# Performance work log

Hardware: AMD Instinct MI355X
Metric: run time of the kernel (lower is better)

Reference implementation:

```python
import jax, jax.numpy as jnp
import numpy as np

# ---- config constants (TwoCompartmentLIFConfig defaults) ----
DT = 1.0                      # ms per Euler step
G_L, E_L = 0.05, 0.0          # somatic leak
G_L_D = 0.03                  # dendritic leak
C_D = 0.5                     # dendritic capacitance
G_C = 0.05                    # soma-dendrite coupling
E_E, E_I = 3.0, -0.5
E_NMDA, E_GABA_B = 3.0, -0.8
E_CA = 4.0
E_ADAPT = -0.5
V_TH, V_RESET, TAU_REF = 1.0, 0.0, 5.0
MG_K, MG_VHALF = 5.0, 0.5     # NMDA Mg2+ block sigmoid
THETA_CA, G_CA_SPIKE = 2.0, 0.3
BAP_AMP = 0.3
ADAPT_INC = 0.0
# conductance decay factors exp(-dt/tau)
D_E  = float(np.exp(-DT / 5.0))
D_I  = float(np.exp(-DT / 10.0))
D_N  = float(np.exp(-DT / 100.0))
D_GB = float(np.exp(-DT / 400.0))
D_CA = float(np.exp(-DT / 20.0))
D_AD = float(np.exp(-DT / 100.0))

T, N = 50, 500000
IN_SCALE = 0.06


def setup_inputs() -> dict:
    key = jax.random.key(0)
    ks = jax.random.split(key, 7)
    names = ["g_exc_basal", "g_inh_basal", "g_nmda_basal", "g_gaba_b_in",
             "g_exc_apical", "g_inh_apical", "g_nmda_apical"]
    return {n: IN_SCALE * jax.random.uniform(k, (T, N), dtype=jnp.float32)
            for n, k in zip(names, ks)}


def _run(g_exc_basal, g_inh_basal, g_nmda_basal, g_gaba_b_in,
         g_exc_apical, g_inh_apical, g_nmda_apical):
    n = g_exc_basal.shape[1]
    z = jnp.zeros((n,), jnp.float32)
    # carry: v_soma, v_dend, gEb, gIb, gNb, gGB, gEa, gIa, gNa, gCa, gAd, ref
    carry0 = (z + E_L, z + E_L, z, z, z, z, z, z, z, z, z, z)

    def step(carry, inp):
        v_s, v_d, gEb, gIb, gNb, gGB, gEa, gIa, gNa, gCa, gAd, ref = carry
        in_Eb, in_Ib, in_Nb, in_GB, in_Ea, in_Ia, in_Na = inp
        # decay + inject synaptic conductances
        gEb = gEb * D_E + in_Eb
        gIb = gIb * D_I + in_Ib
        gNb = gNb * D_N + in_Nb
        gGB = gGB * D_GB + in_GB
        gEa = gEa * D_E + in_Ea
        gIa = gIa * D_I + in_Ia
        gNa = gNa * D_N + in_Na
        gCa = gCa * D_CA
        # NMDA Mg2+ block gated at the LOCAL compartment voltage
        mg_s = jax.nn.sigmoid(MG_K * (v_s - MG_VHALF))
        mg_d = jax.nn.sigmoid(MG_K * (v_d - MG_VHALF))
        # somatic current (C_m = 1)
        I_s = (G_L * (E_L - v_s) + gEb * (E_E - v_s) + gIb * (E_I - v_s)
               + gNb * mg_s * (E_NMDA - v_s) + gGB * (E_GABA_B - v_s)
               + gAd * (E_ADAPT - v_s) + G_C * (v_d - v_s))
        # dendritic current
        I_d = (G_L_D * (E_L - v_d) + gEa * (E_E - v_d) + gIa * (E_I - v_d)
               + gNa * mg_d * (E_NMDA - v_d) + gCa * (E_CA - v_d)
               + G_C * (v_s - v_d))
        refractory = ref > 0.0
        v_s = jnp.where(refractory, V_RESET, v_s + DT * I_s)
        v_d = v_d + (DT / C_D) * I_d
        # spike + reset + refractory
        spike = (v_s >= V_TH) & jnp.logical_not(refractory)
        spike_f = spike.astype(jnp.float32)
        v_s = jnp.where(spike, V_RESET, v_s)
        ref = jnp.where(spike, TAU_REF, jnp.maximum(ref - DT, 0.0))
        gAd = gAd * D_AD + spike_f * ADAPT_INC
        # back-propagating AP depolarises dendrite
        v_d = jnp.where(spike, v_d + BAP_AMP * (E_CA - v_d), v_d)
        # dendritic Ca spike
        gCa = gCa + (v_d >= THETA_CA).astype(jnp.float32) * G_CA_SPIKE
        carry = (v_s, v_d, gEb, gIb, gNb, gGB, gEa, gIa, gNa, gCa, gAd, ref)
        return carry, (spike_f, v_s)

    inputs = (g_exc_basal, g_inh_basal, g_nmda_basal, g_gaba_b_in,
              g_exc_apical, g_inh_apical, g_nmda_apical)
    _, (spikes, v_trace) = jax.lax.scan(step, carry0, inputs)
    return spikes, v_trace  # each [T, N]


def reference(g_exc_basal, g_inh_basal, g_nmda_basal, g_gaba_b_in,
              g_exc_apical, g_inh_apical, g_nmda_apical):
    return _run(g_exc_basal, g_inh_basal, g_nmda_basal, g_gaba_b_in,
                g_exc_apical, g_inh_apical, g_nmda_apical)
```

## Files before the change

kernel.cpp:

```cpp
#include <hip/hip_runtime.h>
#include <math.h>

namespace {
constexpr float D_E   = 0.8187307530779818f;
constexpr float D_I   = 0.9048374180359595f;
constexpr float D_N   = 0.9900498337491681f;
constexpr float D_GB  = 0.9975031223974601f;
constexpr float D_CA  = 0.9512294245007140f;

constexpr float DT      = 1.0f;
constexpr float G_L     = 0.05f;
constexpr float E_L     = 0.0f;
constexpr float G_L_D   = 0.03f;
constexpr float DT_C_D  = 2.0f;
constexpr float G_C     = 0.05f;
constexpr float E_E     = 3.0f;
constexpr float E_I     = -0.5f;
constexpr float E_NMDA  = 3.0f;
constexpr float E_GABA_B= -0.8f;
constexpr float E_CA    = 4.0f;
constexpr float V_TH    = 1.0f;
constexpr float V_RESET = 0.0f;
constexpr float TAU_REF = 5.0f;
constexpr float MG_K    = 5.0f;
constexpr float MG_VHALF= 0.5f;
constexpr float THETA_CA= 2.0f;
constexpr float G_CA_SPIKE = 0.3f;
constexpr float BAP_AMP = 0.3f;
}

typedef float f32x2 __attribute__((ext_vector_type(2)));

__device__ __forceinline__ float fast_sigmoid5(float v) {
    return __fdividef(1.0f, 1.0f + __expf(-MG_K * (v - MG_VHALF)));
}

struct State2 {
    float v_s[2], v_d[2];
    float gEb[2], gIb[2], gNb[2], gGB[2];
    float gEa[2], gIa[2], gNa[2], gCa[2], ref[2];
};

__device__ __forceinline__ void absorb2(
    const f32x2 iEb, const f32x2 iIb, const f32x2 iNb, const f32x2 iGB,
    const f32x2 iEa, const f32x2 iIa, const f32x2 iNa, State2& s)
{
    s.gEb[0] = s.gEb[0]*D_E  + iEb.x;  s.gEb[1] = s.gEb[1]*D_E  + iEb.y;
    s.gIb[0] = s.gIb[0]*D_I  + iIb.x;  s.gIb[1] = s.gIb[1]*D_I  + iIb.y;
    s.gNb[0] = s.gNb[0]*D_N  + iNb.x;  s.gNb[1] = s.gNb[1]*D_N  + iNb.y;
    s.gGB[0] = s.gGB[0]*D_GB + iGB.x;  s.gGB[1] = s.gGB[1]*D_GB + iGB.y;
    s.gEa[0] = s.gEa[0]*D_E  + iEa.x;  s.gEa[1] = s.gEa[1]*D_E  + iEa.y;
    s.gIa[0] = s.gIa[0]*D_I  + iIa.x;  s.gIa[1] = s.gIa[1]*D_I  + iIa.y;
    s.gNa[0] = s.gNa[0]*D_N  + iNa.x;  s.gNa[1] = s.gNa[1]*D_N  + iNa.y;
    s.gCa[0] *= D_CA;                  s.gCa[1] *= D_CA;
}

__device__ __forceinline__ void fire2(State2& s, f32x2& osp, f32x2& ov)
{
    #pragma unroll
    for (int j = 0; j < 2; ++j) {
        float v_s = s.v_s[j], v_d = s.v_d[j];
        const float mg_s = fast_sigmoid5(v_s);
        const float mg_d = fast_sigmoid5(v_d);
        const float I_s = G_L*(E_L - v_s) + s.gEb[j]*(E_E - v_s) + s.gIb[j]*(E_I - v_s)
                        + s.gNb[j]*mg_s*(E_NMDA - v_s) + s.gGB[j]*(E_GABA_B - v_s)
                        + G_C*(v_d - v_s);
        const float I_d = G_L_D*(E_L - v_d) + s.gEa[j]*(E_E - v_d) + s.gIa[j]*(E_I - v_d)
                        + s.gNa[j]*mg_d*(E_NMDA - v_d) + s.gCa[j]*(E_CA - v_d)
                        + G_C*(v_s - v_d);
        const bool refractory = s.ref[j] > 0.0f;
        v_s = refractory ? V_RESET : (v_s + DT*I_s);
        v_d = v_d + DT_C_D*I_d;
        const bool spike = (v_s >= V_TH) && !refractory;
        const float spike_f = spike ? 1.0f : 0.0f;
        v_s = spike ? V_RESET : v_s;
        s.ref[j] = spike ? TAU_REF : fmaxf(s.ref[j] - DT, 0.0f);
        v_d = spike ? (v_d + BAP_AMP*(E_CA - v_d)) : v_d;
        s.gCa[j] += (v_d >= THETA_CA) ? G_CA_SPIKE : 0.0f;
        s.v_s[j] = v_s; s.v_d[j] = v_d;
        if (j == 0) { osp.x = spike_f; ov.x = v_s; }
        else        { osp.y = spike_f; ov.y = v_s; }
    }
}

#define LOAD7(S, OFF)                                     \
    S##Eb = *(const f32x2*)(pEb + (OFF));                 \
    S##Ib = *(const f32x2*)(pIb + (OFF));                 \
    S##Nb = *(const f32x2*)(pNb + (OFF));                 \
    S##GB = *(const f32x2*)(pGB + (OFF));                 \
    S##Ea = *(const f32x2*)(pEa + (OFF));                 \
    S##Ia = *(const f32x2*)(pIa + (OFF));                 \
    S##Na = *(const f32x2*)(pNa + (OFF));

__global__ __launch_bounds__(256, 4)
void lif_f2_pf2_kernel(const float* __restrict__ pEb, const float* __restrict__ pIb,
                       const float* __restrict__ pNb, const float* __restrict__ pGB,
                       const float* __restrict__ pEa, const float* __restrict__ pIa,
                       const float* __restrict__ pNa,
                       float* __restrict__ out, int N, int T)
{
    const int tid = blockIdx.x * blockDim.x + threadIdx.x;
    const long long base = (long long)tid * 2;
    if (base >= N) return;

    State2 s;
    #pragma unroll
    for (int j = 0; j < 2; ++j) {
        s.v_s[j] = E_L; s.v_d[j] = E_L;
        s.gEb[j] = 0; s.gIb[j] = 0; s.gNb[j] = 0; s.gGB[j] = 0;
        s.gEa[j] = 0; s.gIa[j] = 0; s.gNa[j] = 0; s.gCa[j] = 0; s.ref[j] = 0;
    }

    const size_t vtr     = (size_t)T * (size_t)N;
    const size_t lastoff = (size_t)(T - 1) * (size_t)N + (size_t)base;

    size_t off = (size_t)base;
    f32x2 aEb, aIb, aNb, aGB, aEa, aIa, aNa;
    f32x2 bEb, bIb, bNb, bGB, bEa, bIa, bNa;
    LOAD7(a, off)
    LOAD7(b, off + (size_t)N)

    for (int t = 0; t < T; t += 2) {
        f32x2 osp, ov;

        absorb2(aEb, aIb, aNb, aGB, aEa, aIa, aNa, s);
        {
            const size_t la = (t + 2 < T) ? off + 2 * (size_t)N : lastoff;
            LOAD7(a, la)
        }
        fire2(s, osp, ov);
        __builtin_nontemporal_store(osp, reinterpret_cast<f32x2*>(out + off));
        __builtin_nontemporal_store(ov,  reinterpret_cast<f32x2*>(out + vtr + off));
        off += (size_t)N;

        absorb2(bEb, bIb, bNb, bGB, bEa, bIa, bNa, s);
        {
            const size_t lb = (t + 3 < T) ? off + 2 * (size_t)N : lastoff;
            LOAD7(b, lb)
        }
        fire2(s, osp, ov);
        __builtin_nontemporal_store(osp, reinterpret_cast<f32x2*>(out + off));
        __builtin_nontemporal_store(ov,  reinterpret_cast<f32x2*>(out + vtr + off));
        off += (size_t)N;
    }
}

__global__ __launch_bounds__(256, 8)
void lif_scalar_kernel(const float* __restrict__ pEb, const float* __restrict__ pIb,
                       const float* __restrict__ pNb, const float* __restrict__ pGB,
                       const float* __restrict__ pEa, const float* __restrict__ pIa,
                       const float* __restrict__ pNa,
                       float* __restrict__ out, int N, int T)
{
    const int i = blockIdx.x * blockDim.x + threadIdx.x;
    if (i >= N) return;
    State2 s;
    s.v_s[0] = E_L; s.v_d[0] = E_L;
    s.gEb[0] = 0; s.gIb[0] = 0; s.gNb[0] = 0; s.gGB[0] = 0;
    s.gEa[0] = 0; s.gIa[0] = 0; s.gNa[0] = 0; s.gCa[0] = 0; s.ref[0] = 0;
    s.v_s[1] = E_L; s.v_d[1] = E_L;
    s.gEb[1] = 0; s.gIb[1] = 0; s.gNb[1] = 0; s.gGB[1] = 0;
    s.gEa[1] = 0; s.gIa[1] = 0; s.gNa[1] = 0; s.gCa[1] = 0; s.ref[1] = 0;

    const size_t vtr = (size_t)T * (size_t)N;
    for (int t = 0; t < T; ++t) {
        const size_t off = (size_t)t * (size_t)N + (size_t)i;
        f32x2 iEb = {pEb[off], 0.0f}, iIb = {pIb[off], 0.0f};
        f32x2 iNb = {pNb[off], 0.0f}, iGB = {pGB[off], 0.0f};
        f32x2 iEa = {pEa[off], 0.0f}, iIa = {pIa[off], 0.0f};
        f32x2 iNa = {pNa[off], 0.0f};
        absorb2(iEb, iIb, iNb, iGB, iEa, iIa, iNa, s);
        f32x2 osp, ov;
        fire2(s, osp, ov);
        out[off]       = osp.x;
        out[vtr + off] = ov.x;
    }
}

extern "C" void kernel_launch(void* const* d_in, const int* in_sizes, int n_in,
                              void* d_out, int out_size, void* d_ws, size_t ws_size,
                              hipStream_t stream) {
    const float* pEb = (const float*)d_in[0];
    const float* pIb = (const float*)d_in[1];
    const float* pNb = (const float*)d_in[2];
    const float* pGB = (const float*)d_in[3];
    const float* pEa = (const float*)d_in[4];
    const float* pIa = (const float*)d_in[5];
    const float* pNa = (const float*)d_in[6];
    float* out = (float*)d_out;

    const int T = 50;
    const int N = in_sizes[0] / T;

    if ((N & 1) == 0 && (T & 1) == 0) {
        const int threads = N / 2;
        const int blocks = (threads + 255) / 256;
        lif_f2_pf2_kernel<<<blocks, 256, 0, stream>>>(pEb, pIb, pNb, pGB, pEa, pIa, pNa,
                                                      out, N, T);
    } else {
        const int blocks = (N + 255) / 256;
        lif_scalar_kernel<<<blocks, 256, 0, stream>>>(pEb, pIb, pNb, pGB, pEa, pIa, pNa,
                                                      out, N, T);
    }
}
```

Baseline: 174.5 us.

## Stream inputs through double-buffered LDS with direct global-to-LDS loads, 4 neurons per thread

Replaces the register-prefetch float2 kernel with one that issues 16-byte global_load_lds transfers of the next timestep's seven input rows into a double-buffered shared-memory tile, then reads them back as float4. Each thread now handles 4 neurons and writes float4 nontemporal stores. The aim is to raise bytes per memory instruction and let the asynchronous loads overlap compute without using prefetch registers. In exchange it adds a __syncthreads per timestep, drops the occupancy hint to 2 blocks, and clamps the tail block's addresses so lanes past N redundantly recompute and store the last 4 neurons.

```diff
diff --git a/kernel.cpp b/kernel.cpp
--- a/kernel.cpp
+++ b/kernel.cpp
@@ -1,5 +1,6 @@
 #include <hip/hip_runtime.h>
 #include <math.h>
+#include <stdint.h>
 
 namespace {
 constexpr float D_E   = 0.8187307530779818f;
@@ -29,36 +30,39 @@
 constexpr float BAP_AMP = 0.3f;
 }
 
-typedef float f32x2 __attribute__((ext_vector_type(2)));
+typedef float f32x4 __attribute__((ext_vector_type(4)));
 
 __device__ __forceinline__ float fast_sigmoid5(float v) {
     return __fdividef(1.0f, 1.0f + __expf(-MG_K * (v - MG_VHALF)));
 }
 
-struct State2 {
-    float v_s[2], v_d[2];
-    float gEb[2], gIb[2], gNb[2], gGB[2];
-    float gEa[2], gIa[2], gNa[2], gCa[2], ref[2];
+struct State4 {
+    float v_s[4], v_d[4];
+    float gEb[4], gIb[4], gNb[4], gGB[4];
+    float gEa[4], gIa[4], gNa[4], gCa[4], ref[4];
 };
 
-__device__ __forceinline__ void absorb2(
-    const f32x2 iEb, const f32x2 iIb, const f32x2 iNb, const f32x2 iGB,
-    const f32x2 iEa, const f32x2 iIa, const f32x2 iNa, State2& s)
-{
-    s.gEb[0] = s.gEb[0]*D_E  + iEb.x;  s.gEb[1] = s.gEb[1]*D_E  + iEb.y;
-    s.gIb[0] = s.gIb[0]*D_I  + iIb.x;  s.gIb[1] = s.gIb[1]*D_I  + iIb.y;
-    s.gNb[0] = s.gNb[0]*D_N  + iNb.x;  s.gNb[1] = s.gNb[1]*D_N  + iNb.y;
-    s.gGB[0] = s.gGB[0]*D_GB + iGB.x;  s.gGB[1] = s.gGB[1]*D_GB + iGB.y;
-    s.gEa[0] = s.gEa[0]*D_E  + iEa.x;  s.gEa[1] = s.gEa[1]*D_E  + iEa.y;
-    s.gIa[0] = s.gIa[0]*D_I  + iIa.x;  s.gIa[1] = s.gIa[1]*D_I  + iIa.y;
-    s.gNa[0] = s.gNa[0]*D_N  + iNa.x;  s.gNa[1] = s.gNa[1]*D_N  + iNa.y;
-    s.gCa[0] *= D_CA;                  s.gCa[1] *= D_CA;
-}
-
-__device__ __forceinline__ void fire2(State2& s, f32x2& osp, f32x2& ov)
+__device__ __forceinline__ void absorb4(
+    const f32x4 iEb, const f32x4 iIb, const f32x4 iNb, const f32x4 iGB,
+    const f32x4 iEa, const f32x4 iIa, const f32x4 iNa, State4& s)
 {
     #pragma unroll
-    for (int j = 0; j < 2; ++j) {
+    for (int j = 0; j < 4; ++j) {
+        s.gEb[j] = s.gEb[j]*D_E  + iEb[j];
+        s.gIb[j] = s.gIb[j]*D_I  + iIb[j];
+        s.gNb[j] = s.gNb[j]*D_N  + iNb[j];
+        s.gGB[j] = s.gGB[j]*D_GB + iGB[j];
+        s.gEa[j] = s.gEa[j]*D_E  + iEa[j];
+        s.gIa[j] = s.gIa[j]*D_I  + iIa[j];
+        s.gNa[j] = s.gNa[j]*D_N  + iNa[j];
+        s.gCa[j] *= D_CA;
+    }
+}
+
+__device__ __forceinline__ void fire4(State4& s, f32x4& osp, f32x4& ov)
+{
+    #pragma unroll
+    for (int j = 0; j < 4; ++j) {
         float v_s = s.v_s[j], v_d = s.v_d[j];
         const float mg_s = fast_sigmoid5(v_s);
         const float mg_d = fast_sigmoid5(v_d);
@@ -78,70 +82,77 @@
         v_d = spike ? (v_d + BAP_AMP*(E_CA - v_d)) : v_d;
         s.gCa[j] += (v_d >= THETA_CA) ? G_CA_SPIKE : 0.0f;
         s.v_s[j] = v_s; s.v_d[j] = v_d;
-        if (j == 0) { osp.x = spike_f; ov.x = v_s; }
-        else        { osp.y = spike_f; ov.y = v_s; }
-    }
-}
-
-#define LOAD7(S, OFF)                                     \
-    S##Eb = *(const f32x2*)(pEb + (OFF));                 \
-    S##Ib = *(const f32x2*)(pIb + (OFF));                 \
-    S##Nb = *(const f32x2*)(pNb + (OFF));                 \
-    S##GB = *(const f32x2*)(pGB + (OFF));                 \
-    S##Ea = *(const f32x2*)(pEa + (OFF));                 \
-    S##Ia = *(const f32x2*)(pIa + (OFF));                 \
-    S##Na = *(const f32x2*)(pNa + (OFF));
-
-__global__ __launch_bounds__(256, 4)
-void lif_f2_pf2_kernel(const float* __restrict__ pEb, const float* __restrict__ pIb,
-                       const float* __restrict__ pNb, const float* __restrict__ pGB,
-                       const float* __restrict__ pEa, const float* __restrict__ pIa,
-                       const float* __restrict__ pNa,
-                       float* __restrict__ out, int N, int T)
-{
-    const int tid = blockIdx.x * blockDim.x + threadIdx.x;
-    const long long base = (long long)tid * 2;
-    if (base >= N) return;
-
-    State2 s;
+        osp[j] = spike_f; ov[j] = v_s;
+    }
+}
+
+__global__ __launch_bounds__(256, 2)
+void lif_lds_kernel(const float* __restrict__ pEb, const float* __restrict__ pIb,
+                    const float* __restrict__ pNb, const float* __restrict__ pGB,
+                    const float* __restrict__ pEa, const float* __restrict__ pIa,
+                    const float* __restrict__ pNa,
+                    float* __restrict__ outSp, float* __restrict__ outV,
+                    int N, int T)
+{
+    __shared__ float lds[2][7][1024];
+    const int tid  = threadIdx.x;
+    const int wave = tid >> 6;
+    const float* in[7] = {pEb, pIb, pNb, pGB, pEa, pIa, pNa};
+
+    const long long b0  = (long long)blockIdx.x * 1024 + (long long)tid * 4;
+    const long long nm4 = (long long)N - 4;
+    const size_t gb = (size_t)(b0 < nm4 ? b0 : nm4);
+
+    {
+        #pragma unroll
+        for (int a = 0; a < 7; ++a)
+            __builtin_amdgcn_global_load_lds(
+                (const __attribute__((address_space(1))) uint32_t*)(in[a] + gb),
+                (__attribute__((address_space(3))) uint32_t*)&lds[0][a][wave * 256],
+                16, 0, 0);
+    }
+
+    State4 s;
     #pragma unroll
-    for (int j = 0; j < 2; ++j) {
+    for (int j = 0; j < 4; ++j) {
         s.v_s[j] = E_L; s.v_d[j] = E_L;
         s.gEb[j] = 0; s.gIb[j] = 0; s.gNb[j] = 0; s.gGB[j] = 0;
         s.gEa[j] = 0; s.gIa[j] = 0; s.gNa[j] = 0; s.gCa[j] = 0; s.ref[j] = 0;
     }
 
-    const size_t vtr     = (size_t)T * (size_t)N;
-    const size_t lastoff = (size_t)(T - 1) * (size_t)N + (size_t)base;
-
-    size_t off = (size_t)base;
-    f32x2 aEb, aIb, aNb, aGB, aEa, aIa, aNa;
-    f32x2 bEb, bIb, bNb, bGB, bEa, bIa, bNa;
-    LOAD7(a, off)
-    LOAD7(b, off + (size_t)N)
-
-    for (int t = 0; t < T; t += 2) {
-        f32x2 osp, ov;
-
-        absorb2(aEb, aIb, aNb, aGB, aEa, aIa, aNa, s);
-        {
-            const size_t la = (t + 2 < T) ? off + 2 * (size_t)N : lastoff;
-            LOAD7(a, la)
+    __syncthreads();
+
+    for (int t = 0; t < T; ++t) {
+        const int cur = t & 1;
+
+        if (t + 1 < T) {
+            const size_t row = (size_t)(t + 1) * (size_t)N + gb;
+            #pragma unroll
+            for (int a = 0; a < 7; ++a)
+                __builtin_amdgcn_global_load_lds(
+                    (const __attribute__((address_space(1))) uint32_t*)(in[a] + row),
+                    (__attribute__((address_space(3))) uint32_t*)&lds[cur ^ 1][a][wave * 256],
+                    16, 0, 0);
         }
-        fire2(s, osp, ov);
-        __builtin_nontemporal_store(osp, reinterpret_cast<f32x2*>(out + off));
-        __builtin_nontemporal_store(ov,  reinterpret_cast<f32x2*>(out + vtr + off));
-        off += (size_t)N;
-
-        absorb2(bEb, bIb, bNb, bGB, bEa, bIa, bNa, s);
-        {
-            const size_t lb = (t + 3 < T) ? off + 2 * (size_t)N : lastoff;
-            LOAD7(b, lb)
-        }
-        fire2(s, osp, ov);
-        __builtin_nontemporal_store(osp, reinterpret_cast<f32x2*>(out + off));
-        __builtin_nontemporal_store(ov,  reinterpret_cast<f32x2*>(out + vtr + off));
-        off += (size_t)N;
+
+        const int li = tid * 4;
+        const f32x4 iEb = *(const f32x4*)&lds[cur][0][li];
+        const f32x4 iIb = *(const f32x4*)&lds[cur][1][li];
+        const f32x4 iNb = *(const f32x4*)&lds[cur][2][li];
+        const f32x4 iGB = *(const f32x4*)&lds[cur][3][li];
+        const f32x4 iEa = *(const f32x4*)&lds[cur][4][li];
+        const f32x4 iIa = *(const f32x4*)&lds[cur][5][li];
+        const f32x4 iNa = *(const f32x4*)&lds[cur][6][li];
+
+        absorb4(iEb, iIb, iNb, iGB, iEa, iIa, iNa, s);
+        f32x4 osp, ov;
+        fire4(s, osp, ov);
+
+        const size_t o = (size_t)t * (size_t)N + gb;
+        __builtin_nontemporal_store(osp, (f32x4*)(outSp + o));
+        __builtin_nontemporal_store(ov,  (f32x4*)(outV  + o));
+
+        __syncthreads();
     }
 }
 
@@ -154,26 +165,40 @@
 {
     const int i = blockIdx.x * blockDim.x + threadIdx.x;
     if (i >= N) return;
-    State2 s;
-    s.v_s[0] = E_L; s.v_d[0] = E_L;
-    s.gEb[0] = 0; s.gIb[0] = 0; s.gNb[0] = 0; s.gGB[0] = 0;
-    s.gEa[0] = 0; s.gIa[0] = 0; s.gNa[0] = 0; s.gCa[0] = 0; s.ref[0] = 0;
-    s.v_s[1] = E_L; s.v_d[1] = E_L;
-    s.gEb[1] = 0; s.gIb[1] = 0; s.gNb[1] = 0; s.gGB[1] = 0;
-    s.gEa[1] = 0; s.gIa[1] = 0; s.gNa[1] = 0; s.gCa[1] = 0; s.ref[1] = 0;
-
+
+    float v_s = E_L, v_d = E_L;
+    float gEb = 0, gIb = 0, gNb = 0, gGB = 0;
+    float gEa = 0, gIa = 0, gNa = 0, gCa = 0, ref = 0;
     const size_t vtr = (size_t)T * (size_t)N;
+
     for (int t = 0; t < T; ++t) {
         const size_t off = (size_t)t * (size_t)N + (size_t)i;
-        f32x2 iEb = {pEb[off], 0.0f}, iIb = {pIb[off], 0.0f};
-        f32x2 iNb = {pNb[off], 0.0f}, iGB = {pGB[off], 0.0f};
-        f32x2 iEa = {pEa[off], 0.0f}, iIa = {pIa[off], 0.0f};
-        f32x2 iNa = {pNa[off], 0.0f};
-        absorb2(iEb, iIb, iNb, iGB, iEa, iIa, iNa, s);
-        f32x2 osp, ov;
-        fire2(s, osp, ov);
-        out[off]       = osp.x;
-        out[vtr + off] = ov.x;
+        gEb = gEb*D_E  + pEb[off];
+        gIb = gIb*D_I  + pIb[off];
+        gNb = gNb*D_N  + pNb[off];
+        gGB = gGB*D_GB + pGB[off];
+        gEa = gEa*D_E  + pEa[off];
+        gIa = gIa*D_I  + pIa[off];
+        gNa = gNa*D_N  + pNa[off];
+        gCa *= D_CA;
+        const float mg_s = fast_sigmoid5(v_s);
+        const float mg_d = fast_sigmoid5(v_d);
+        const float I_s = G_L*(E_L - v_s) + gEb*(E_E - v_s) + gIb*(E_I - v_s)
+                        + gNb*mg_s*(E_NMDA - v_s) + gGB*(E_GABA_B - v_s)
+                        + G_C*(v_d - v_s);
+        const float I_d = G_L_D*(E_L - v_d) + gEa*(E_E - v_d) + gIa*(E_I - v_d)
+                        + gNa*mg_d*(E_NMDA - v_d) + gCa*(E_CA - v_d)
+                        + G_C*(v_s - v_d);
+        const bool refractory = ref > 0.0f;
+        v_s = refractory ? V_RESET : (v_s + DT*I_s);
+        v_d = v_d + DT_C_D*I_d;
+        const bool spike = (v_s >= V_TH) && !refractory;
+        v_s = spike ? V_RESET : v_s;
+        ref = spike ? TAU_REF : fmaxf(ref - DT, 0.0f);
+        v_d = spike ? (v_d + BAP_AMP*(E_CA - v_d)) : v_d;
+        gCa += (v_d >= THETA_CA) ? G_CA_SPIKE : 0.0f;
+        out[off]       = spike ? 1.0f : 0.0f;
+        out[vtr + off] = v_s;
     }
 }
 
@@ -192,11 +217,11 @@
     const int T = 50;
     const int N = in_sizes[0] / T;
 
-    if ((N & 1) == 0 && (T & 1) == 0) {
-        const int threads = N / 2;
-        const int blocks = (threads + 255) / 256;
-        lif_f2_pf2_kernel<<<blocks, 256, 0, stream>>>(pEb, pIb, pNb, pGB, pEa, pIa, pNa,
-                                                      out, N, T);
+    if ((N & 3) == 0 && N >= 4) {
+        const int blocks = (N + 1023) / 1024;
+        float* outV = out + (size_t)T * (size_t)N;
+        lif_lds_kernel<<<blocks, 256, 0, stream>>>(pEb, pIb, pNb, pGB, pEa, pIa, pNa,
+                                                   out, outV, N, T);
     } else {
         const int blocks = (N + 255) / 256;
         lif_scalar_kernel<<<blocks, 256, 0, stream>>>(pEb, pIb, pNb, pGB, pEa, pIa, pNa,
```

New measurement: 171.8 us. About the same (-1.6%).
